# Optimization experiments

Measured on AMD Instinct MI355X. Metric: run time of the kernel, lower is better.

The kernel has to match this reference:

```python
import jax, jax.numpy as jnp
import numpy as np

ALPHA = 0.2        # LeakyReLU negative slope
NEG = -9e15        # mask value used by the torch module
N, FIN, H, D = 4096, 20, 4, 64


def gat_layer(h, adj_mask, W, a_src, a_dst, average):
    """Multi-head GAT layer. W: [H,Fin,Fout], a_src/a_dst: [H,Fout].
    e_ij = LeakyReLU(a_src . Wh_i + a_dst . Wh_j) == a^T [Wh_i || Wh_j],
    identical math to the N x N x 2F concat in the torch code, without
    materializing the pairwise concat tensor."""
    Wh = jnp.einsum('nf,hfo->hno', h, W)                 # [H,N,F]
    f_s = jnp.einsum('hno,ho->hn', Wh, a_src)            # [H,N]
    f_d = jnp.einsum('hno,ho->hn', Wh, a_dst)            # [H,N]
    e = jax.nn.leaky_relu(f_s[:, :, None] + f_d[:, None, :], ALPHA)  # [H,N,N]
    e = jnp.where(adj_mask[None], e, NEG)
    att = jax.nn.softmax(e, axis=-1)
    out = jax.nn.elu(jnp.einsum('hnm,hmo->hno', att, Wh))  # per-head ELU (concat=True inside)
    if average:
        return out.mean(axis=0)                           # [N,F]
    return jnp.transpose(out, (1, 0, 2)).reshape(h.shape[0], -1)  # [N,H*F]


def setup_inputs() -> dict:
    key = jax.random.key(0)
    ks = jax.random.split(key, 6)
    x = jax.random.normal(ks[0], (N, FIN), jnp.float32)
    adj = jax.random.randint(ks[1], (N, N), 0, 2, jnp.int32)
    # layer 0: 20 -> 64 per head, 4 heads, concat -> 256
    W0 = jax.random.normal(ks[2], (H, FIN, D), jnp.float32) * 0.3
    a0 = jax.random.normal(ks[3], (H, 2 * D), jnp.float32) * 0.1
    # layer 1: 256 -> 64 per head, heads averaged
    W1 = jax.random.normal(ks[4], (H, H * D, D), jnp.float32) * 0.06
    a1 = jax.random.normal(ks[5], (H, 2 * D), jnp.float32) * 0.1
    return {"x": x, "adj": adj, "W0": W0, "a0": a0, "W1": W1, "a1": a1}


def reference(x, adj, W0, a0, W1, a1):
    mask = adj > 0
    h = gat_layer(x, mask, W0, a0[:, :D], a0[:, D:], average=False)   # [N, 256]
    return gat_layer(h, mask, W1, a1[:, :D], a1[:, D:], average=True)  # [N, 64]
```

## Files before the change

kernel.cpp:

```cpp
#include <hip/hip_runtime.h>
#include <hip/hip_fp16.h>
#include <math.h>

#define NN 4096
#define FIN 20
#define NH 4
#define DH 64
#define ALPHA 0.2f
#define LOG2E 1.4426950408889634f

typedef _Float16 f16x8 __attribute__((ext_vector_type(8)));
typedef _Float16 f16x4 __attribute__((ext_vector_type(4)));
typedef __fp16 fp16x2 __attribute__((ext_vector_type(2)));
typedef float f32x4 __attribute__((ext_vector_type(4)));

__device__ inline void gload_lds16(const void* gsrc, void* ldsbase) {
    __builtin_amdgcn_global_load_lds(
        (const __attribute__((address_space(1))) void*)gsrc,
        (__attribute__((address_space(3))) void*)ldsbase, 16, 0, 0);
}

__global__ __launch_bounds__(256) void k_front(const int* __restrict__ adj,
        unsigned char* __restrict__ bits, const float* __restrict__ x,
        const float* __restrict__ W0, const float* __restrict__ a0,
        _Float16* __restrict__ whT, float* __restrict__ fs, float* __restrict__ fd,
        const float* __restrict__ W1, _Float16* __restrict__ w1T) {
    __shared__ float xs[16 * FIN];
    const int bid = blockIdx.x;
    const int tid = threadIdx.x;
    if (bid < 8192) {
        int t = bid * 256 + tid;
        const int4* p = (const int4*)(adj + (size_t)t * 8);
        int4 a = p[0], b = p[1];
        unsigned int byte = 0;
        byte |= (a.x > 0) << 0; byte |= (a.y > 0) << 1;
        byte |= (a.z > 0) << 2; byte |= (a.w > 0) << 3;
        byte |= (b.x > 0) << 4; byte |= (b.y > 0) << 5;
        byte |= (b.z > 0) << 6; byte |= (b.w > 0) << 7;
        bits[t] = (unsigned char)byte;
    } else if (bid < 8448) {
        int n0 = (bid - 8192) * 16;
        for (int i = tid; i < 16 * FIN; i += 256) xs[i] = x[n0 * FIN + i];
        __syncthreads();
        int h = tid >> 6, d = tid & 63;
        float w0r[FIN];
#pragma unroll
        for (int f = 0; f < FIN; ++f) w0r[f] = W0[(h * FIN + f) * DH + d];
        float asrc = a0[h * 2 * DH + d];
        float adst = a0[h * 2 * DH + DH + d];
        f16x8 wv[2];
#pragma unroll
        for (int n = 0; n < 16; ++n) {
            float wh = 0.f;
#pragma unroll
            for (int f = 0; f < FIN; ++f) wh = fmaf(xs[n * FIN + f], w0r[f], wh);
            wv[n >> 3][n & 7] = (_Float16)wh;
            float sv = wh * asrc, dv = wh * adst;
#pragma unroll
            for (int off = 1; off <= 32; off <<= 1) {
                sv += __shfl_xor(sv, off);
                dv += __shfl_xor(dv, off);
            }
            if (d == 0) { fs[h * NN + n0 + n] = sv; fd[h * NN + n0 + n] = dv; }
        }
        _Float16* dst = whT + ((size_t)(h * DH + d) * NN + n0);
        *(f16x8*)(dst) = wv[0];
        *(f16x8*)(dst + 8) = wv[1];
    } else {
        int u = (bid - 8448) * 256 + tid;
        int h = u >> 14, f = (u >> 6) & 255, d = u & 63;
        w1T[((size_t)(h * DH + d) << 8) + f] = (_Float16)W1[u];
    }
}

__global__ __launch_bounds__(256) void k_fdmax(const float* __restrict__ fd,
        float* __restrict__ fdm) {
    int h = blockIdx.x, tid = threadIdx.x;
    float m = -3e38f;
    for (int i = tid; i < NN; i += 256) m = fmaxf(m, fd[h * NN + i]);
#pragma unroll
    for (int off = 1; off <= 32; off <<= 1) m = fmaxf(m, __shfl_xor(m, off));
    __shared__ float mx[4];
    if ((tid & 63) == 0) mx[tid >> 6] = m;
    __syncthreads();
    if (tid == 0) fdm[h] = fmaxf(fmaxf(mx[0], mx[1]), fmaxf(mx[2], mx[3]));
}

__global__ __launch_bounds__(512) void k_attn(const float* __restrict__ fs,
        const float* __restrict__ fd, const float* __restrict__ fdmax,
        const _Float16* __restrict__ whT, const unsigned char* __restrict__ bits,
        float* __restrict__ pv, float* __restrict__ pl) {
    __shared__ __align__(16) char smem[34304];
    const int ch = blockIdx.x & 1;
    const int rowblk = (blockIdx.x >> 1) & 63;
    const int h = blockIdx.x >> 7;
    const int row0 = rowblk << 6;
    const int cb0 = ch << 11;
    const int tid = threadIdx.x;
    const int l = tid & 63, w = tid >> 6;
    const int rl = l & 15, g = l >> 4;
    const int rg = w >> 2, cq = w & 3;
    const int r0 = row0 + rg * 32 + rl;
    const int r1 = r0 + 16;
    const float fsr0 = fs[h * NN + r0], fsr1 = fs[h * NN + r1];
    const float fm = fdmax[h];
    const float su0 = fsr0 + fm, su1 = fsr1 + fm;
    const float m0 = fmaxf(su0, ALPHA * su0);
    const float m1 = fmaxf(su1, ALPHA * su1);
    const float A0 = (fsr0 - m0) * LOG2E, B0 = (ALPHA * fsr0 - m0) * LOG2E;
    const float A1 = (fsr1 - m1) * LOG2E, B1 = (ALPHA * fsr1 - m1) * LOG2E;
    const float* fdp = fd + h * NN + cb0 + cq * 32 + g * 8;
    const unsigned char* bp0 = bits + (size_t)r0 * (NN / 8) + (cb0 >> 3) + cq * 4;
    const unsigned char* bp1 = bits + (size_t)r1 * (NN / 8) + (cb0 >> 3) + cq * 4;
    const _Float16* whb = whT + (size_t)h * DH * NN + cb0;

    const int d0_ = tid >> 4, c0_ = tid & 15;
    const int d1_ = (512 + tid) >> 4, c1_ = tid & 15;
    const _Float16* src0 = whb + (size_t)d0_ * NN + 8 * (c0_ ^ (d0_ & 7));
    const _Float16* src1 = whb + (size_t)d1_ * NN + 8 * (c1_ ^ (d1_ & 7));

    f32x4 acc0[4] = {{0,0,0,0},{0,0,0,0},{0,0,0,0},{0,0,0,0}};
    f32x4 acc1[4] = {{0,0,0,0},{0,0,0,0},{0,0,0,0},{0,0,0,0}};
    f32x4 al0 = {0,0,0,0}, al1 = {0,0,0,0};
    f16x8 ones;
#pragma unroll
    for (int i = 0; i < 8; ++i) ones[i] = (_Float16)1.0f;
    const int rdswz = (cq * 64 + g * 16) ^ ((rl & 7) << 4);

    float4 faA, fbA, faB, fbB;
    unsigned int mA0, mA1, mB0, mB1;

#define STAGE(BOFF, T)                                                          \
    gload_lds16(src0 + (T) * 128, smem + (BOFF) + w * 1024);                    \
    gload_lds16(src1 + (T) * 128, smem + (BOFF) + 8192 + w * 1024);

#define FEED(FA, FB, M0v, M1v, T)                                               \
    FA = *(const float4*)(fdp + (T) * 128);                                     \
    FB = *(const float4*)(fdp + (T) * 128 + 4);                                 \
    M0v = *(const unsigned int*)(bp0 + (T) * 16);                               \
    M1v = *(const unsigned int*)(bp1 + (T) * 16);

#define COMPUTE(BOFF, FA, FB, M0v, M1v)                                         \
    {                                                                           \
        const char* buf_ = smem + (BOFF);                                       \
        const float fv[8] = {FA.x, FA.y, FA.z, FA.w, FB.x, FB.y, FB.z, FB.w};   \
        f16x8 av0, av1;                                                         \
        const int sh = g << 3;                                                  \
        _Pragma("unroll")                                                       \
        for (int i = 0; i < 8; i += 2) {                                        \
            float ta = fmaxf(fmaf(fv[i], LOG2E, A0), fmaf(fv[i], ALPHA * LOG2E, B0)); \
            ta = ((M0v >> (sh + i)) & 1u) ? ta : -1e30f;                        \
            float tb = fmaxf(fmaf(fv[i+1], LOG2E, A0), fmaf(fv[i+1], ALPHA * LOG2E, B0)); \
            tb = ((M0v >> (sh + i + 1)) & 1u) ? tb : -1e30f;                    \
            fp16x2 p0 = __builtin_amdgcn_cvt_pkrtz(exp2f(ta), exp2f(tb));       \
            av0[i] = (_Float16)p0[0]; av0[i+1] = (_Float16)p0[1];               \
            float tc = fmaxf(fmaf(fv[i], LOG2E, A1), fmaf(fv[i], ALPHA * LOG2E, B1)); \
            tc = ((M1v >> (sh + i)) & 1u) ? tc : -1e30f;                        \
            float td = fmaxf(fmaf(fv[i+1], LOG2E, A1), fmaf(fv[i+1], ALPHA * LOG2E, B1)); \
            td = ((M1v >> (sh + i + 1)) & 1u) ? td : -1e30f;                    \
            fp16x2 p1 = __builtin_amdgcn_cvt_pkrtz(exp2f(tc), exp2f(td));       \
            av1[i] = (_Float16)p1[0]; av1[i+1] = (_Float16)p1[1];               \
        }                                                                       \
        al0 = __builtin_amdgcn_mfma_f32_16x16x32_f16(av0, ones, al0, 0, 0, 0);  \
        al1 = __builtin_amdgcn_mfma_f32_16x16x32_f16(av1, ones, al1, 0, 0, 0);  \
        _Pragma("unroll")                                                       \
        for (int t4 = 0; t4 < 4; ++t4) {                                        \
            f16x8 bv = *(const f16x8*)(buf_ + ((16 * t4 + rl) << 8) + rdswz);   \
            acc0[t4] = __builtin_amdgcn_mfma_f32_16x16x32_f16(av0, bv, acc0[t4], 0, 0, 0); \
            acc1[t4] = __builtin_amdgcn_mfma_f32_16x16x32_f16(av1, bv, acc1[t4], 0, 0, 0); \
        }                                                                       \
    }

#define WAIT6 asm volatile("s_waitcnt vmcnt(6)" ::: "memory");                  \
    __builtin_amdgcn_s_barrier();                                               \
    __builtin_amdgcn_sched_barrier(0);

    STAGE(0, 0);      FEED(faA, fbA, mA0, mA1, 0);
    STAGE(16384, 1);  FEED(faB, fbB, mB0, mB1, 1);

#pragma unroll 1
    for (int k = 0; k < 7; ++k) {
        WAIT6
        COMPUTE(0, faA, fbA, mA0, mA1);
        __builtin_amdgcn_s_barrier();
        STAGE(0, 2 * k + 2);  FEED(faA, fbA, mA0, mA1, 2 * k + 2);
        WAIT6
        COMPUTE(16384, faB, fbB, mB0, mB1);
        __builtin_amdgcn_s_barrier();
        STAGE(16384, 2 * k + 3);  FEED(faB, fbB, mB0, mB1, 2 * k + 3);
    }
    WAIT6
    COMPUTE(0, faA, fbA, mA0, mA1);
    asm volatile("s_waitcnt vmcnt(0)" ::: "memory");
    __builtin_amdgcn_s_barrier();
    __builtin_amdgcn_sched_barrier(0);
    COMPUTE(16384, faB, fbB, mB0, mB1);
    __syncthreads();
#undef WAIT6
#undef COMPUTE
#undef FEED
#undef STAGE

    float* red = (float*)smem;
    float* lred = (float*)(smem + 33792);
#pragma unroll
    for (int p = 0; p < 2; ++p) {
        if (rg == p) {
#pragma unroll
            for (int t4 = 0; t4 < 4; ++t4)
#pragma unroll
                for (int i = 0; i < 4; ++i) {
                    red[(cq * 32 + 4 * g + i) * 66 + 16 * t4 + rl]      = acc0[t4][i];
                    red[(cq * 32 + 16 + 4 * g + i) * 66 + 16 * t4 + rl] = acc1[t4][i];
                }
            if (rl == 0) {
#pragma unroll
                for (int i = 0; i < 4; ++i) {
                    lred[cq * 32 + 4 * g + i]      = al0[i];
                    lred[cq * 32 + 16 + 4 * g + i] = al1[i];
                }
            }
        }
        __syncthreads();
#pragma unroll
        for (int j = 0; j < 4; ++j) {
            const int R = w * 4 + j;
            float v = 0.f, L = 0.f;
#pragma unroll
            for (int cc = 0; cc < 4; ++cc) {
                v += red[(cc * 32 + R) * 66 + l];
                L += lred[cc * 32 + R];
            }
            const int Rg = row0 + p * 32 + R;
            pv[(((size_t)(ch * NH + h) * NN) + Rg) * 64 + l] = v;
            if (l == 0) pl[(size_t)(ch * NH + h) * NN + Rg] = L;
        }
        __syncthreads();
    }
}

template<int MODE>
__global__ __launch_bounds__(256) void k_merge(const float* __restrict__ pv,
        const float* __restrict__ pl, void* __restrict__ outp) {
    int t = blockIdx.x * 256 + threadIdx.x;
    if (MODE == 0) {
        int d = t & 63, n = (t >> 6) & (NN - 1), h = t >> 18;
        float v = pv[((size_t)h * NN + n) * 64 + d] + pv[((size_t)(NH + h) * NN + n) * 64 + d];
        float L = pl[h * NN + n] + pl[NH * NN + h * NN + n];
        float o = v * __builtin_amdgcn_rcpf(L);
        o = o > 0.f ? o : __expf(o) - 1.f;
        ((_Float16*)outp)[(size_t)n * (NH * DH) + h * DH + d] = (_Float16)o;
    } else {
        int d = t & 63, n = t >> 6;
        float s = 0.f;
#pragma unroll
        for (int h = 0; h < NH; ++h) {
            float v = pv[((size_t)h * NN + n) * 64 + d] + pv[((size_t)(NH + h) * NN + n) * 64 + d];
            float L = pl[h * NN + n] + pl[NH * NN + h * NN + n];
            float o = v * __builtin_amdgcn_rcpf(L);
            s += o > 0.f ? o : __expf(o) - 1.f;
        }
        ((float*)outp)[t] = 0.25f * s;
    }
}

__global__ __launch_bounds__(256) void k_l1wh(const _Float16* __restrict__ h16,
        const _Float16* __restrict__ w1T, const float* __restrict__ a1,
        _Float16* __restrict__ whT, float* __restrict__ fs, float* __restrict__ fd) {
    __shared__ float red[4][16][64];
    __shared__ _Float16 lt[16][64];
    int h = blockIdx.x >> 8;
    int row0 = (blockIdx.x & 255) << 4;
    int tid = threadIdx.x;
    int l = tid & 63, w = tid >> 6;
    int rl = l & 15, g = l >> 4;
    f32x4 acc[4] = {{0,0,0,0},{0,0,0,0},{0,0,0,0},{0,0,0,0}};
    const _Float16* ap = h16 + (size_t)(row0 + rl) * (NH * DH) + w * 64;
    const _Float16* bp = w1T + ((size_t)h * DH << 8) + w * 64;
#pragma unroll
    for (int j = 0; j < 2; ++j) {
        int fb = j * 32 + 8 * g;
        f16x8 avv = *(const f16x8*)(ap + fb);
#pragma unroll
        for (int t4 = 0; t4 < 4; ++t4) {
            f16x8 bv = *(const f16x8*)(bp + ((size_t)(16 * t4 + rl) << 8) + fb);
            acc[t4] = __builtin_amdgcn_mfma_f32_16x16x32_f16(avv, bv, acc[t4], 0, 0, 0);
        }
    }
#pragma unroll
    for (int t4 = 0; t4 < 4; ++t4)
#pragma unroll
        for (int i = 0; i < 4; ++i) red[w][t4 * 4 + i][l] = acc[t4][i];
    __syncthreads();
#pragma unroll
    for (int i = 0; i < 4; ++i) {
        float v = red[0][w * 4 + i][l] + red[1][w * 4 + i][l]
                + red[2][w * 4 + i][l] + red[3][w * 4 + i][l];
        lt[4 * g + i][16 * w + rl] = (_Float16)v;
    }
    __syncthreads();
    int d = tid & 63, rb = tid >> 6;
    f16x4 o;
#pragma unroll
    for (int j = 0; j < 4; ++j) o[j] = lt[rb * 4 + j][d];
    *(f16x4*)(whT + (size_t)(h * DH + d) * NN + row0 + rb * 4) = o;
    float as_ = a1[h * 2 * DH + d], ad_ = a1[h * 2 * DH + DH + d];
    float svj[4], dvj[4];
#pragma unroll
    for (int j = 0; j < 4; ++j) {
        float wv = (float)lt[rb * 4 + j][d];
        svj[j] = wv * as_;
        dvj[j] = wv * ad_;
    }
#pragma unroll
    for (int off = 1; off <= 32; off <<= 1) {
#pragma unroll
        for (int j = 0; j < 4; ++j) {
            svj[j] += __shfl_xor(svj[j], off);
            dvj[j] += __shfl_xor(dvj[j], off);
        }
    }
    if (d == 0) {
#pragma unroll
        for (int j = 0; j < 4; ++j) {
            fs[h * NN + row0 + rb * 4 + j] = svj[j];
            fd[h * NN + row0 + rb * 4 + j] = dvj[j];
        }
    }
}

extern "C" void kernel_launch(void* const* d_in, const int* in_sizes, int n_in,
                              void* d_out, int out_size, void* d_ws, size_t ws_size,
                              hipStream_t stream) {
    const float* x  = (const float*)d_in[0];
    const int* adj  = (const int*)d_in[1];
    const float* W0 = (const float*)d_in[2];
    const float* a0 = (const float*)d_in[3];
    const float* W1 = (const float*)d_in[4];
    const float* a1 = (const float*)d_in[5];
    float* out = (float*)d_out;
    char* ws = (char*)d_ws;

    unsigned char* bits = (unsigned char*)(ws);
    _Float16* whT0 = (_Float16*)(ws + (2ull << 20));
    _Float16* h16  = (_Float16*)(ws + (4ull << 20));
    _Float16* w1T  = (_Float16*)(ws + (6ull << 20));
    _Float16* whT1 = (_Float16*)(ws + (6ull << 20) + (256ull << 10));
    float* fs0  = (float*)(ws + (9ull << 20));
    float* fd0  = fs0 + NH * NN;
    float* fs1  = fd0 + NH * NN;
    float* fd1  = fs1 + NH * NN;
    float* fdm0 = fd1 + NH * NN;
    float* fdm1 = fdm0 + 8;
    float* pv   = (float*)(ws + (10ull << 20));
    float* pl   = (float*)(ws + (18ull << 20));

    k_front<<<8704, 256, 0, stream>>>(adj, bits, x, W0, a0, whT0, fs0, fd0, W1, w1T);
    k_fdmax<<<NH, 256, 0, stream>>>(fd0, fdm0);
    k_attn<<<2 * NH * (NN / 64), 512, 0, stream>>>(fs0, fd0, fdm0, whT0, bits, pv, pl);
    k_merge<0><<<(NH * NN * DH) / 256, 256, 0, stream>>>(pv, pl, h16);
    k_l1wh<<<NH * (NN / 16), 256, 0, stream>>>(h16, w1T, a1, whT1, fs1, fd1);
    k_fdmax<<<NH, 256, 0, stream>>>(fd1, fdm1);
    k_attn<<<2 * NH * (NN / 64), 512, 0, stream>>>(fs1, fd1, fdm1, whT1, bits, pv, pl);
    k_merge<1><<<(NN * DH) / 256, 256, 0, stream>>>(pv, pl, out);
}
```

Measured before the change: 134.0 us.

## Factor softmax exponentials into per-row and per-column precomputed terms

Adds a k_prep kernel that precomputes exp(fs+fm-m), exp(alpha*(fs+fm)-m), exp(fd-fm) and exp(alpha*(fd-fm)) per node. The attention inner loop then forms each weight as max(E*F, E'*F') with two multiplies instead of two exp2 calls, which removes the transcendental work from the N×N loop. The cost is two extra feed loads per tile, a deeper vmcnt wait, and an extra kernel launch per layer. It also changes the LDS swizzle pattern. There is a risk of fp32 underflow or overflow in the factored products.

After: 152.0 us. 13.4% more time.

```diff
diff --git a/kernel.cpp b/kernel.cpp
--- a/kernel.cpp
+++ b/kernel.cpp
@@ -7,7 +7,6 @@
 #define NH 4
 #define DH 64
 #define ALPHA 0.2f
-#define LOG2E 1.4426950408889634f
 
 typedef _Float16 f16x8 __attribute__((ext_vector_type(8)));
 typedef _Float16 f16x4 __attribute__((ext_vector_type(4)));
@@ -86,9 +85,26 @@
     if (tid == 0) fdm[h] = fmaxf(fmaxf(mx[0], mx[1]), fmaxf(mx[2], mx[3]));
 }
 
-__global__ __launch_bounds__(512) void k_attn(const float* __restrict__ fs,
-        const float* __restrict__ fd, const float* __restrict__ fdmax,
-        const _Float16* __restrict__ whT, const unsigned char* __restrict__ bits,
+__global__ __launch_bounds__(256) void k_prep(const float* __restrict__ fs,
+        const float* __restrict__ fd, const float* __restrict__ fdm,
+        float* __restrict__ E, float* __restrict__ Ep,
+        float* __restrict__ F, float* __restrict__ Fp) {
+    int u = blockIdx.x * 256 + threadIdx.x;
+    int h = u >> 12;
+    float fm = fdm[h];
+    float dv = fd[u] - fm;
+    F[u]  = __expf(dv);
+    Fp[u] = __expf(ALPHA * dv);
+    float su = fs[u] + fm;
+    float m = fmaxf(su, ALPHA * su);
+    E[u]  = __expf(su - m);
+    Ep[u] = __expf(ALPHA * su - m);
+}
+
+__global__ __launch_bounds__(512) void k_attn(const float* __restrict__ E,
+        const float* __restrict__ Ep, const float* __restrict__ F,
+        const float* __restrict__ Fp, const _Float16* __restrict__ whT,
+        const unsigned char* __restrict__ bits,
         float* __restrict__ pv, float* __restrict__ pl) {
     __shared__ __align__(16) char smem[34304];
     const int ch = blockIdx.x & 1;
@@ -102,22 +118,18 @@
     const int rg = w >> 2, cq = w & 3;
     const int r0 = row0 + rg * 32 + rl;
     const int r1 = r0 + 16;
-    const float fsr0 = fs[h * NN + r0], fsr1 = fs[h * NN + r1];
-    const float fm = fdmax[h];
-    const float su0 = fsr0 + fm, su1 = fsr1 + fm;
-    const float m0 = fmaxf(su0, ALPHA * su0);
-    const float m1 = fmaxf(su1, ALPHA * su1);
-    const float A0 = (fsr0 - m0) * LOG2E, B0 = (ALPHA * fsr0 - m0) * LOG2E;
-    const float A1 = (fsr1 - m1) * LOG2E, B1 = (ALPHA * fsr1 - m1) * LOG2E;
-    const float* fdp = fd + h * NN + cb0 + cq * 32 + g * 8;
+    const float E0  = E[h * NN + r0],  E1  = E[h * NN + r1];
+    const float E0p = Ep[h * NN + r0], E1p = Ep[h * NN + r1];
+    const float* Fq  = F  + h * NN + cb0 + cq * 32 + g * 8;
+    const float* Fpq = Fp + h * NN + cb0 + cq * 32 + g * 8;
     const unsigned char* bp0 = bits + (size_t)r0 * (NN / 8) + (cb0 >> 3) + cq * 4;
     const unsigned char* bp1 = bits + (size_t)r1 * (NN / 8) + (cb0 >> 3) + cq * 4;
     const _Float16* whb = whT + (size_t)h * DH * NN + cb0;
 
     const int d0_ = tid >> 4, c0_ = tid & 15;
-    const int d1_ = (512 + tid) >> 4, c1_ = tid & 15;
-    const _Float16* src0 = whb + (size_t)d0_ * NN + 8 * (c0_ ^ (d0_ & 7));
-    const _Float16* src1 = whb + (size_t)d1_ * NN + 8 * (c1_ ^ (d1_ & 7));
+    const int d1_ = 32 + (tid >> 4), c1_ = tid & 15;
+    const _Float16* src0 = whb + (size_t)d0_ * NN + 8 * (c0_ ^ (d0_ & 15));
+    const _Float16* src1 = whb + (size_t)d1_ * NN + 8 * (c1_ ^ (d1_ & 15));
 
     f32x4 acc0[4] = {{0,0,0,0},{0,0,0,0},{0,0,0,0},{0,0,0,0}};
     f32x4 acc1[4] = {{0,0,0,0},{0,0,0,0},{0,0,0,0},{0,0,0,0}};
@@ -125,40 +137,43 @@
     f16x8 ones;
 #pragma unroll
     for (int i = 0; i < 8; ++i) ones[i] = (_Float16)1.0f;
-    const int rdswz = (cq * 64 + g * 16) ^ ((rl & 7) << 4);
-
-    float4 faA, fbA, faB, fbB;
+    const int rdswz = ((((cq << 2) | g) ^ rl) << 4);
+
+    float4 faA, fbA, fpaA, fpbA, faB, fbB, fpaB, fpbB;
     unsigned int mA0, mA1, mB0, mB1;
 
 #define STAGE(BOFF, T)                                                          \
     gload_lds16(src0 + (T) * 128, smem + (BOFF) + w * 1024);                    \
     gload_lds16(src1 + (T) * 128, smem + (BOFF) + 8192 + w * 1024);
 
-#define FEED(FA, FB, M0v, M1v, T)                                               \
-    FA = *(const float4*)(fdp + (T) * 128);                                     \
-    FB = *(const float4*)(fdp + (T) * 128 + 4);                                 \
+#define FEED(FA, FB, FPA, FPB, M0v, M1v, T)                                     \
+    FA  = *(const float4*)(Fq  + (T) * 128);                                    \
+    FB  = *(const float4*)(Fq  + (T) * 128 + 4);                                \
+    FPA = *(const float4*)(Fpq + (T) * 128);                                    \
+    FPB = *(const float4*)(Fpq + (T) * 128 + 4);                                \
     M0v = *(const unsigned int*)(bp0 + (T) * 16);                               \
     M1v = *(const unsigned int*)(bp1 + (T) * 16);
 
-#define COMPUTE(BOFF, FA, FB, M0v, M1v)                                         \
+#define COMPUTE(BOFF, FA, FB, FPA, FPB, M0v, M1v)                               \
     {                                                                           \
         const char* buf_ = smem + (BOFF);                                       \
         const float fv[8] = {FA.x, FA.y, FA.z, FA.w, FB.x, FB.y, FB.z, FB.w};   \
+        const float fp[8] = {FPA.x, FPA.y, FPA.z, FPA.w, FPB.x, FPB.y, FPB.z, FPB.w}; \
         f16x8 av0, av1;                                                         \
         const int sh = g << 3;                                                  \
         _Pragma("unroll")                                                       \
         for (int i = 0; i < 8; i += 2) {                                        \
-            float ta = fmaxf(fmaf(fv[i], LOG2E, A0), fmaf(fv[i], ALPHA * LOG2E, B0)); \
-            ta = ((M0v >> (sh + i)) & 1u) ? ta : -1e30f;                        \
-            float tb = fmaxf(fmaf(fv[i+1], LOG2E, A0), fmaf(fv[i+1], ALPHA * LOG2E, B0)); \
-            tb = ((M0v >> (sh + i + 1)) & 1u) ? tb : -1e30f;                    \
-            fp16x2 p0 = __builtin_amdgcn_cvt_pkrtz(exp2f(ta), exp2f(tb));       \
+            float ta = fmaxf(E0 * fv[i], E0p * fp[i]);                          \
+            ta = ((M0v >> (sh + i)) & 1u) ? ta : 0.f;                           \
+            float tb = fmaxf(E0 * fv[i+1], E0p * fp[i+1]);                      \
+            tb = ((M0v >> (sh + i + 1)) & 1u) ? tb : 0.f;                       \
+            fp16x2 p0 = __builtin_amdgcn_cvt_pkrtz(ta, tb);                     \
             av0[i] = (_Float16)p0[0]; av0[i+1] = (_Float16)p0[1];               \
-            float tc = fmaxf(fmaf(fv[i], LOG2E, A1), fmaf(fv[i], ALPHA * LOG2E, B1)); \
-            tc = ((M1v >> (sh + i)) & 1u) ? tc : -1e30f;                        \
-            float td = fmaxf(fmaf(fv[i+1], LOG2E, A1), fmaf(fv[i+1], ALPHA * LOG2E, B1)); \
-            td = ((M1v >> (sh + i + 1)) & 1u) ? td : -1e30f;                    \
-            fp16x2 p1 = __builtin_amdgcn_cvt_pkrtz(exp2f(tc), exp2f(td));       \
+            float tc = fmaxf(E1 * fv[i], E1p * fp[i]);                          \
+            tc = ((M1v >> (sh + i)) & 1u) ? tc : 0.f;                           \
+            float td = fmaxf(E1 * fv[i+1], E1p * fp[i+1]);                      \
+            td = ((M1v >> (sh + i + 1)) & 1u) ? td : 0.f;                       \
+            fp16x2 p1 = __builtin_amdgcn_cvt_pkrtz(tc, td);                     \
             av1[i] = (_Float16)p1[0]; av1[i+1] = (_Float16)p1[1];               \
         }                                                                       \
         al0 = __builtin_amdgcn_mfma_f32_16x16x32_f16(av0, ones, al0, 0, 0, 0);  \
@@ -171,32 +186,32 @@
         }                                                                       \
     }
 
-#define WAIT6 asm volatile("s_waitcnt vmcnt(6)" ::: "memory");                  \
+#define WAIT8 asm volatile("s_waitcnt vmcnt(8)" ::: "memory");                  \
     __builtin_amdgcn_s_barrier();                                               \
     __builtin_amdgcn_sched_barrier(0);
 
-    STAGE(0, 0);      FEED(faA, fbA, mA0, mA1, 0);
-    STAGE(16384, 1);  FEED(faB, fbB, mB0, mB1, 1);
+    STAGE(0, 0);      FEED(faA, fbA, fpaA, fpbA, mA0, mA1, 0);
+    STAGE(16384, 1);  FEED(faB, fbB, fpaB, fpbB, mB0, mB1, 1);
 
 #pragma unroll 1
     for (int k = 0; k < 7; ++k) {
-        WAIT6
-        COMPUTE(0, faA, fbA, mA0, mA1);
+        WAIT8
+        COMPUTE(0, faA, fbA, fpaA, fpbA, mA0, mA1);
         __builtin_amdgcn_s_barrier();
-        STAGE(0, 2 * k + 2);  FEED(faA, fbA, mA0, mA1, 2 * k + 2);
-        WAIT6
-        COMPUTE(16384, faB, fbB, mB0, mB1);
+        STAGE(0, 2 * k + 2);  FEED(faA, fbA, fpaA, fpbA, mA0, mA1, 2 * k + 2);
+        WAIT8
+        COMPUTE(16384, faB, fbB, fpaB, fpbB, mB0, mB1);
         __builtin_amdgcn_s_barrier();
-        STAGE(16384, 2 * k + 3);  FEED(faB, fbB, mB0, mB1, 2 * k + 3);
-    }
-    WAIT6
-    COMPUTE(0, faA, fbA, mA0, mA1);
+        STAGE(16384, 2 * k + 3);  FEED(faB, fbB, fpaB, fpbB, mB0, mB1, 2 * k + 3);
+    }
+    WAIT8
+    COMPUTE(0, faA, fbA, fpaA, fpbA, mA0, mA1);
     asm volatile("s_waitcnt vmcnt(0)" ::: "memory");
     __builtin_amdgcn_s_barrier();
     __builtin_amdgcn_sched_barrier(0);
-    COMPUTE(16384, faB, fbB, mB0, mB1);
+    COMPUTE(16384, faB, fbB, fpaB, fpbB, mB0, mB1);
     __syncthreads();
-#undef WAIT6
+#undef WAIT8
 #undef COMPUTE
 #undef FEED
 #undef STAGE
@@ -354,13 +369,19 @@
     float* fdm1 = fdm0 + 8;
     float* pv   = (float*)(ws + (10ull << 20));
     float* pl   = (float*)(ws + (18ull << 20));
+    float* Ea   = (float*)(ws + (19ull << 20));
+    float* Epa  = Ea + NH * NN;
+    float* Fa   = Epa + NH * NN;
+    float* Fpa  = Fa + NH * NN;
 
     k_front<<<8704, 256, 0, stream>>>(adj, bits, x, W0, a0, whT0, fs0, fd0, W1, w1T);
     k_fdmax<<<NH, 256, 0, stream>>>(fd0, fdm0);
-    k_attn<<<2 * NH * (NN / 64), 512, 0, stream>>>(fs0, fd0, fdm0, whT0, bits, pv, pl);
+    k_prep<<<NH * NN / 256, 256, 0, stream>>>(fs0, fd0, fdm0, Ea, Epa, Fa, Fpa);
+    k_attn<<<2 * NH * (NN / 64), 512, 0, stream>>>(Ea, Epa, Fa, Fpa, whT0, bits, pv, pl);
     k_merge<0><<<(NH * NN * DH) / 256, 256, 0, stream>>>(pv, pl, h16);
     k_l1wh<<<NH * (NN / 16), 256, 0, stream>>>(h16, w1T, a1, whT1, fs1, fd1);
     k_fdmax<<<NH, 256, 0, stream>>>(fd1, fdm1);
-    k_attn<<<2 * NH * (NN / 64), 512, 0, stream>>>(fs1, fd1, fdm1, whT1, bits, pv, pl);
+    k_prep<<<NH * NN / 256, 256, 0, stream>>>(fs1, fd1, fdm1, Ea, Epa, Fa, Fpa);
+    k_attn<<<2 * NH * (NN / 64), 512, 0, stream>>>(Ea, Epa, Fa, Fpa, whT1, bits, pv, pl);
     k_merge<1><<<(NN * DH) / 256, 256, 0, stream>>>(pv, pl, out);
 }
```

## Halve attention row tile to 32 rows per block, doubling grid size

Applied to the files above, without the earlier changes.

The attention kernel now handles 32 query rows per block instead of 64. Each wave computes one 16-row MFMA tile instead of two, and the grid doubles to 1024 blocks. The shared-memory swizzle and the vmcnt wait count are adjusted to match, and the two-pass cross-wave reduction collapses into a single pass. The aim is more blocks in flight and fewer live registers per thread. The cost is that each staged Wh tile and fd vector is reused across half as many rows, so global and L2 traffic for them doubles.

New measurement: 140.7 us. +4.9%, slower.

```diff
diff --git a/kernel.cpp b/kernel.cpp
--- a/kernel.cpp
+++ b/kernel.cpp
@@ -92,59 +92,53 @@
         float* __restrict__ pv, float* __restrict__ pl) {
     __shared__ __align__(16) char smem[34304];
     const int ch = blockIdx.x & 1;
-    const int rowblk = (blockIdx.x >> 1) & 63;
-    const int h = blockIdx.x >> 7;
-    const int row0 = rowblk << 6;
+    const int rowblk = (blockIdx.x >> 1) & 127;
+    const int h = blockIdx.x >> 8;
+    const int row0 = rowblk << 5;
     const int cb0 = ch << 11;
     const int tid = threadIdx.x;
     const int l = tid & 63, w = tid >> 6;
     const int rl = l & 15, g = l >> 4;
-    const int rg = w >> 2, cq = w & 3;
-    const int r0 = row0 + rg * 32 + rl;
-    const int r1 = r0 + 16;
-    const float fsr0 = fs[h * NN + r0], fsr1 = fs[h * NN + r1];
+    const int cq = w & 3, rg = w >> 2;
+    const int r0 = row0 + rg * 16 + rl;
+    const float fsr = fs[h * NN + r0];
     const float fm = fdmax[h];
-    const float su0 = fsr0 + fm, su1 = fsr1 + fm;
-    const float m0 = fmaxf(su0, ALPHA * su0);
-    const float m1 = fmaxf(su1, ALPHA * su1);
-    const float A0 = (fsr0 - m0) * LOG2E, B0 = (ALPHA * fsr0 - m0) * LOG2E;
-    const float A1 = (fsr1 - m1) * LOG2E, B1 = (ALPHA * fsr1 - m1) * LOG2E;
+    const float su = fsr + fm;
+    const float m0 = fmaxf(su, ALPHA * su);
+    const float A0 = (fsr - m0) * LOG2E, B0 = (ALPHA * fsr - m0) * LOG2E;
     const float* fdp = fd + h * NN + cb0 + cq * 32 + g * 8;
     const unsigned char* bp0 = bits + (size_t)r0 * (NN / 8) + (cb0 >> 3) + cq * 4;
-    const unsigned char* bp1 = bits + (size_t)r1 * (NN / 8) + (cb0 >> 3) + cq * 4;
     const _Float16* whb = whT + (size_t)h * DH * NN + cb0;
 
     const int d0_ = tid >> 4, c0_ = tid & 15;
-    const int d1_ = (512 + tid) >> 4, c1_ = tid & 15;
-    const _Float16* src0 = whb + (size_t)d0_ * NN + 8 * (c0_ ^ (d0_ & 7));
-    const _Float16* src1 = whb + (size_t)d1_ * NN + 8 * (c1_ ^ (d1_ & 7));
-
-    f32x4 acc0[4] = {{0,0,0,0},{0,0,0,0},{0,0,0,0},{0,0,0,0}};
-    f32x4 acc1[4] = {{0,0,0,0},{0,0,0,0},{0,0,0,0},{0,0,0,0}};
-    f32x4 al0 = {0,0,0,0}, al1 = {0,0,0,0};
+    const int d1_ = 32 + (tid >> 4), c1_ = tid & 15;
+    const _Float16* src0 = whb + (size_t)d0_ * NN + 8 * (c0_ ^ (d0_ & 15));
+    const _Float16* src1 = whb + (size_t)d1_ * NN + 8 * (c1_ ^ (d1_ & 15));
+
+    f32x4 acc[4] = {{0,0,0,0},{0,0,0,0},{0,0,0,0},{0,0,0,0}};
+    f32x4 al = {0,0,0,0};
     f16x8 ones;
 #pragma unroll
     for (int i = 0; i < 8; ++i) ones[i] = (_Float16)1.0f;
-    const int rdswz = (cq * 64 + g * 16) ^ ((rl & 7) << 4);
+    const int rdswz = ((((cq << 2) | g) ^ rl) << 4);
 
     float4 faA, fbA, faB, fbB;
-    unsigned int mA0, mA1, mB0, mB1;
+    unsigned int mA0, mB0;
 
 #define STAGE(BOFF, T)                                                          \
     gload_lds16(src0 + (T) * 128, smem + (BOFF) + w * 1024);                    \
     gload_lds16(src1 + (T) * 128, smem + (BOFF) + 8192 + w * 1024);
 
-#define FEED(FA, FB, M0v, M1v, T)                                               \
+#define FEED(FA, FB, M0v, T)                                                    \
     FA = *(const float4*)(fdp + (T) * 128);                                     \
     FB = *(const float4*)(fdp + (T) * 128 + 4);                                 \
-    M0v = *(const unsigned int*)(bp0 + (T) * 16);                               \
-    M1v = *(const unsigned int*)(bp1 + (T) * 16);
-
-#define COMPUTE(BOFF, FA, FB, M0v, M1v)                                         \
+    M0v = *(const unsigned int*)(bp0 + (T) * 16);
+
+#define COMPUTE(BOFF, FA, FB, M0v)                                              \
     {                                                                           \
         const char* buf_ = smem + (BOFF);                                       \
         const float fv[8] = {FA.x, FA.y, FA.z, FA.w, FB.x, FB.y, FB.z, FB.w};   \
-        f16x8 av0, av1;                                                         \
+        f16x8 av;                                                               \
         const int sh = g << 3;                                                  \
         _Pragma("unroll")                                                       \
         for (int i = 0; i < 8; i += 2) {                                        \
@@ -153,50 +147,42 @@
             float tb = fmaxf(fmaf(fv[i+1], LOG2E, A0), fmaf(fv[i+1], ALPHA * LOG2E, B0)); \
             tb = ((M0v >> (sh + i + 1)) & 1u) ? tb : -1e30f;                    \
             fp16x2 p0 = __builtin_amdgcn_cvt_pkrtz(exp2f(ta), exp2f(tb));       \
-            av0[i] = (_Float16)p0[0]; av0[i+1] = (_Float16)p0[1];               \
-            float tc = fmaxf(fmaf(fv[i], LOG2E, A1), fmaf(fv[i], ALPHA * LOG2E, B1)); \
-            tc = ((M1v >> (sh + i)) & 1u) ? tc : -1e30f;                        \
-            float td = fmaxf(fmaf(fv[i+1], LOG2E, A1), fmaf(fv[i+1], ALPHA * LOG2E, B1)); \
-            td = ((M1v >> (sh + i + 1)) & 1u) ? td : -1e30f;                    \
-            fp16x2 p1 = __builtin_amdgcn_cvt_pkrtz(exp2f(tc), exp2f(td));       \
-            av1[i] = (_Float16)p1[0]; av1[i+1] = (_Float16)p1[1];               \
+            av[i] = (_Float16)p0[0]; av[i+1] = (_Float16)p0[1];                 \
         }                                                                       \
-        al0 = __builtin_amdgcn_mfma_f32_16x16x32_f16(av0, ones, al0, 0, 0, 0);  \
-        al1 = __builtin_amdgcn_mfma_f32_16x16x32_f16(av1, ones, al1, 0, 0, 0);  \
+        al = __builtin_amdgcn_mfma_f32_16x16x32_f16(av, ones, al, 0, 0, 0);     \
         _Pragma("unroll")                                                       \
         for (int t4 = 0; t4 < 4; ++t4) {                                        \
             f16x8 bv = *(const f16x8*)(buf_ + ((16 * t4 + rl) << 8) + rdswz);   \
-            acc0[t4] = __builtin_amdgcn_mfma_f32_16x16x32_f16(av0, bv, acc0[t4], 0, 0, 0); \
-            acc1[t4] = __builtin_amdgcn_mfma_f32_16x16x32_f16(av1, bv, acc1[t4], 0, 0, 0); \
+            acc[t4] = __builtin_amdgcn_mfma_f32_16x16x32_f16(av, bv, acc[t4], 0, 0, 0); \
         }                                                                       \
     }
 
-#define WAIT6 asm volatile("s_waitcnt vmcnt(6)" ::: "memory");                  \
+#define WAIT5 asm volatile("s_waitcnt vmcnt(5)" ::: "memory");                  \
     __builtin_amdgcn_s_barrier();                                               \
     __builtin_amdgcn_sched_barrier(0);
 
-    STAGE(0, 0);      FEED(faA, fbA, mA0, mA1, 0);
-    STAGE(16384, 1);  FEED(faB, fbB, mB0, mB1, 1);
+    STAGE(0, 0);      FEED(faA, fbA, mA0, 0);
+    STAGE(16384, 1);  FEED(faB, fbB, mB0, 1);
 
 #pragma unroll 1
     for (int k = 0; k < 7; ++k) {
-        WAIT6
-        COMPUTE(0, faA, fbA, mA0, mA1);
+        WAIT5
+        COMPUTE(0, faA, fbA, mA0);
         __builtin_amdgcn_s_barrier();
-        STAGE(0, 2 * k + 2);  FEED(faA, fbA, mA0, mA1, 2 * k + 2);
-        WAIT6
-        COMPUTE(16384, faB, fbB, mB0, mB1);
+        STAGE(0, 2 * k + 2);  FEED(faA, fbA, mA0, 2 * k + 2);
+        WAIT5
+        COMPUTE(16384, faB, fbB, mB0);
         __builtin_amdgcn_s_barrier();
-        STAGE(16384, 2 * k + 3);  FEED(faB, fbB, mB0, mB1, 2 * k + 3);
-    }
-    WAIT6
-    COMPUTE(0, faA, fbA, mA0, mA1);
+        STAGE(16384, 2 * k + 3);  FEED(faB, fbB, mB0, 2 * k + 3);
+    }
+    WAIT5
+    COMPUTE(0, faA, fbA, mA0);
     asm volatile("s_waitcnt vmcnt(0)" ::: "memory");
     __builtin_amdgcn_s_barrier();
     __builtin_amdgcn_sched_barrier(0);
-    COMPUTE(16384, faB, fbB, mB0, mB1);
-    __syncthreads();
-#undef WAIT6
+    COMPUTE(16384, faB, fbB, mB0);
+    __syncthreads();
+#undef WAIT5
 #undef COMPUTE
 #undef FEED
 #undef STAGE
@@ -204,38 +190,28 @@
     float* red = (float*)smem;
     float* lred = (float*)(smem + 33792);
 #pragma unroll
-    for (int p = 0; p < 2; ++p) {
-        if (rg == p) {
-#pragma unroll
-            for (int t4 = 0; t4 < 4; ++t4)
-#pragma unroll
-                for (int i = 0; i < 4; ++i) {
-                    red[(cq * 32 + 4 * g + i) * 66 + 16 * t4 + rl]      = acc0[t4][i];
-                    red[(cq * 32 + 16 + 4 * g + i) * 66 + 16 * t4 + rl] = acc1[t4][i];
-                }
-            if (rl == 0) {
-#pragma unroll
-                for (int i = 0; i < 4; ++i) {
-                    lred[cq * 32 + 4 * g + i]      = al0[i];
-                    lred[cq * 32 + 16 + 4 * g + i] = al1[i];
-                }
-            }
-        }
-        __syncthreads();
-#pragma unroll
-        for (int j = 0; j < 4; ++j) {
-            const int R = w * 4 + j;
-            float v = 0.f, L = 0.f;
-#pragma unroll
-            for (int cc = 0; cc < 4; ++cc) {
-                v += red[(cc * 32 + R) * 66 + l];
-                L += lred[cc * 32 + R];
-            }
-            const int Rg = row0 + p * 32 + R;
-            pv[(((size_t)(ch * NH + h) * NN) + Rg) * 64 + l] = v;
-            if (l == 0) pl[(size_t)(ch * NH + h) * NN + Rg] = L;
-        }
-        __syncthreads();
+    for (int t4 = 0; t4 < 4; ++t4)
+#pragma unroll
+        for (int i = 0; i < 4; ++i)
+            red[(cq * 32 + rg * 16 + 4 * g + i) * 66 + 16 * t4 + rl] = acc[t4][i];
+    if (rl == 0) {
+#pragma unroll
+        for (int i = 0; i < 4; ++i)
+            lred[cq * 32 + rg * 16 + 4 * g + i] = al[i];
+    }
+    __syncthreads();
+#pragma unroll
+    for (int j = 0; j < 4; ++j) {
+        const int R = w * 4 + j;
+        float v = 0.f, L = 0.f;
+#pragma unroll
+        for (int cc = 0; cc < 4; ++cc) {
+            v += red[(cc * 32 + R) * 66 + l];
+            L += lred[cc * 32 + R];
+        }
+        const int Rg = row0 + R;
+        pv[(((size_t)(ch * NH + h) * NN) + Rg) * 64 + l] = v;
+        if (l == 0) pl[(size_t)(ch * NH + h) * NN + Rg] = L;
     }
 }
 
@@ -357,10 +333,10 @@
 
     k_front<<<8704, 256, 0, stream>>>(adj, bits, x, W0, a0, whT0, fs0, fd0, W1, w1T);
     k_fdmax<<<NH, 256, 0, stream>>>(fd0, fdm0);
-    k_attn<<<2 * NH * (NN / 64), 512, 0, stream>>>(fs0, fd0, fdm0, whT0, bits, pv, pl);
+    k_attn<<<2 * NH * (NN / 32), 512, 0, stream>>>(fs0, fd0, fdm0, whT0, bits, pv, pl);
     k_merge<0><<<(NH * NN * DH) / 256, 256, 0, stream>>>(pv, pl, h16);
     k_l1wh<<<NH * (NN / 16), 256, 0, stream>>>(h16, w1T, a1, whT1, fs1, fd1);
     k_fdmax<<<NH, 256, 0, stream>>>(fd1, fdm1);
-    k_attn<<<2 * NH * (NN / 64), 512, 0, stream>>>(fs1, fd1, fdm1, whT1, bits, pv, pl);
+    k_attn<<<2 * NH * (NN / 32), 512, 0, stream>>>(fs1, fd1, fdm1, whT1, bits, pv, pl);
     k_merge<1><<<(NN * DH) / 256, 256, 0, stream>>>(pv, pl, out);
 }
```
